# Kernel tuning notes

Measured on AMD Instinct MI355X. Metric: run time of the kernel, lower is better.

Reference implementation:

```python
import jax, jax.numpy as jnp
import numpy as np

SH_DEGREE = 1
D_SH = (SH_DEGREE + 1) ** 2  # 4
SCALE_MIN = 0.5
SCALE_MAX = 15.0
MULTIPLIER = 0.1
EPS = 1e-8


def quat_to_rotmat(q):
    # q: [..., 4] (w, x, y, z), assumed (near-)normalized
    w, x, y, z = q[..., 0], q[..., 1], q[..., 2], q[..., 3]
    return jnp.stack([
        jnp.stack([1 - 2 * (y * y + z * z), 2 * (x * y - w * z), 2 * (x * z + w * y)], -1),
        jnp.stack([2 * (x * y + w * z), 1 - 2 * (x * x + z * z), 2 * (y * z - w * x)], -1),
        jnp.stack([2 * (x * z - w * y), 2 * (y * z + w * x), 1 - 2 * (x * x + y * y)], -1),
    ], -2)


def setup_inputs() -> dict:
    key = jax.random.key(0)
    ks = jax.random.split(key, 6)
    B, N = 8, 131072
    H, W = 256, 512
    # valid SE(3) extrinsics (rotation from random unit quaternion)
    q = jax.random.normal(ks[0], (B, 1, 4), dtype=jnp.float32)
    q = q / jnp.linalg.norm(q, axis=-1, keepdims=True)
    R = quat_to_rotmat(q)
    t = jax.random.normal(ks[1], (B, 1, 3), dtype=jnp.float32)
    ext = jnp.zeros((B, 1, 4, 4), jnp.float32)
    ext = ext.at[..., :3, :3].set(R).at[..., :3, 3].set(t).at[..., 3, 3].set(1.0)
    # normalized pinhole intrinsics
    K = jnp.array([[1.2, 0.0, 0.5], [0.0, 1.2, 0.5], [0.0, 0.0, 1.0]], jnp.float32)
    K = jnp.broadcast_to(K, (B, 1, 3, 3))
    coordinates = jax.random.uniform(ks[2], (B, N, 2), dtype=jnp.float32)
    depths = jax.random.uniform(ks[3], (B, N), dtype=jnp.float32, minval=0.5, maxval=10.0)
    opacities = jax.random.uniform(ks[4], (B, N), dtype=jnp.float32)
    raw_gaussians = jax.random.normal(ks[5], (B, N, 7 + 3 * D_SH), dtype=jnp.float32)
    return {"extrinsics": ext, "intrinsics": K, "coordinates": coordinates,
            "depths": depths, "opacities": opacities, "raw_gaussians": raw_gaussians,
            "h": H, "w": W}


def reference(extrinsics, intrinsics, coordinates, depths, opacities, raw_gaussians, h, w):
    # sh mask: degree-0 untouched, degree d scaled by 0.1 * 0.25**d
    sh_mask = jnp.ones((D_SH,), jnp.float32)
    for d in range(1, SH_DEGREE + 1):
        sh_mask = sh_mask.at[d ** 2:(d + 1) ** 2].set(0.1 * 0.25 ** d)

    scales_raw = raw_gaussians[..., :3]
    rot_raw = raw_gaussians[..., 3:7]
    sh = raw_gaussians[..., 7:]

    scales = SCALE_MIN + (SCALE_MAX - SCALE_MIN) * jax.nn.sigmoid(scales_raw)

    # scale multiplier from inverse of 2x2 top-left of intrinsics
    pixel_size = 1.0 / jnp.array([w, h], jnp.float32)
    a = intrinsics[..., 0, 0]; b = intrinsics[..., 0, 1]
    c = intrinsics[..., 1, 0]; d = intrinsics[..., 1, 1]
    det = a * d - b * c
    inv2 = jnp.stack([jnp.stack([d, -b], -1), jnp.stack([-c, a], -1)], -2) / det[..., None, None]
    multiplier = (MULTIPLIER * jnp.einsum('...ij,j->...i', inv2, pixel_size)).sum(-1)  # [B,1]

    scales = scales * depths[..., None] * multiplier[..., None]  # [B,N,3]

    rotations = rot_raw / (jnp.linalg.norm(rot_raw, axis=-1, keepdims=True) + EPS)  # [B,N,4]

    sh = sh.reshape(*sh.shape[:-1], 3, D_SH) * sh_mask  # [B,N,3,D_SH]

    # covariance = R diag(s^2) R^T, then rotate into world frame
    R = quat_to_rotmat(rotations)  # [B,N,3,3]
    cov = jnp.einsum('...ij,...j,...kj->...ik', R, scales * scales, R)
    c2w = extrinsics[..., :3, :3]  # [B,1,3,3]
    cov = jnp.einsum('...ij,...jk,...lk->...il', c2w, cov, c2w)  # [B,N,3,3]

    # world rays: unproject pixel coords with depth 1, normalize, rotate to world
    coords_h = jnp.concatenate([coordinates, jnp.ones_like(coordinates[..., :1])], -1)  # [B,N,3]
    Kinv = jnp.linalg.inv(intrinsics)  # [B,1,3,3]
    dirs = jnp.einsum('...ij,...j->...i', Kinv, coords_h)
    dirs = dirs / jnp.linalg.norm(dirs, axis=-1, keepdims=True)
    dirs_w = jnp.einsum('...ij,...j->...i', c2w, dirs)  # [B,N,3]
    origins = jnp.broadcast_to(extrinsics[..., :3, 3], dirs_w.shape)
    means = origins + dirs_w * depths[..., None]  # [B,N,3]

    # rotate SH: l=0 identity; l=1 Wigner-D equals c2w in the (y,z,x) permuted basis
    p = jnp.array([1, 2, 0])
    D1 = c2w[..., p, :][..., :, p]  # [B,1,3,3]
    sh0 = sh[..., :1]
    sh1 = jnp.einsum('...ij,...cj->...ci', D1, sh[..., 1:4])
    harmonics = jnp.concatenate([sh0, sh1], -1)  # [B,N,3,D_SH]

    rotations_b = jnp.broadcast_to(rotations, (*scales.shape[:-1], 4))
    return (means, cov, harmonics, opacities, scales, rotations_b)
```

## Files before the change

kernel.cpp:

```cpp
#include <hip/hip_runtime.h>
#include <math.h>

#define SCALE_MIN 0.5f
#define SCALE_MAX 15.0f
#define MULTIPLIER 0.1f
#define EPS 1e-8f

typedef float v4f __attribute__((ext_vector_type(4)));
typedef float v2f __attribute__((ext_vector_type(2)));


#define WVF 1216
#define A_MEAN  0
#define A_COV   192
#define A_SCALE 768

__global__ __launch_bounds__(256, 4) void mono_gaussian_adapter_kernel(
    const float* __restrict__ ext,
    const float* __restrict__ intr,
    const float* __restrict__ coord,
    const float* __restrict__ depth,
    const float* __restrict__ opac,
    const float* __restrict__ rawg,
    const int* __restrict__ hp,
    const int* __restrict__ wp,
    float* __restrict__ out,
    int bpb,
    int BN)
{
    __shared__ __align__(16) float lds[4 * WVF];

    const int tid  = threadIdx.x;
    const int lane = tid & 63;
    const int wid  = tid >> 6;
    const int blk  = blockIdx.x;
    const int gid  = blk * 256 + tid;
    const int gw   = blk * 4 + wid;
    const int b    = blk / bpb;

    float* lw = lds + wid * WVF;

    {
        const v4f* gsrc = (const v4f*)(rawg + (long long)gw * (64 * 19));
        #pragma unroll
        for (int i = 0; i < 4; ++i) {
            __builtin_amdgcn_global_load_lds(
                (const __attribute__((address_space(1))) void*)(gsrc + i * 64 + lane),
                (__attribute__((address_space(3))) void*)((v4f*)lw + i * 64),
                16, 0, 0);
        }
        if (lane < 48) {
            __builtin_amdgcn_global_load_lds(
                (const __attribute__((address_space(1))) void*)(gsrc + 256 + lane),
                (__attribute__((address_space(3))) void*)((v4f*)lw + 256),
                16, 0, 0);
        }
    }

    v2f uv  = __builtin_nontemporal_load((const v2f*)coord + gid);
    float dep = __builtin_nontemporal_load(depth + gid);
    float op  = __builtin_nontemporal_load(opac + gid);

    float inv_w = 1.0f / (float)wp[0];
    float inv_h = 1.0f / (float)hp[0];

    const float* E = ext + b * 16;
    float c00=E[0],  c01=E[1],  c02=E[2],  t0=E[3];
    float c10=E[4],  c11=E[5],  c12=E[6],  t1=E[7];
    float c20=E[8],  c21=E[9],  c22=E[10], t2=E[11];

    const float* Kb = intr + b * 9;
    float k00=Kb[0],k01=Kb[1],k02=Kb[2];
    float k10=Kb[3],k11=Kb[4],k12=Kb[5];
    float k20=Kb[6],k21=Kb[7],k22=Kb[8];

    float det2 = k00*k11 - k01*k10;
    float mult = MULTIPLIER * ((k11*inv_w - k01*inv_h) + (k00*inv_h - k10*inv_w)) / det2;

    float det3 = k00*(k11*k22 - k12*k21)
               + k01*(k12*k20 - k10*k22)
               + k02*(k10*k21 - k11*k20);
    float id3 = 1.0f / det3;
    float i00 = (k11*k22 - k12*k21)*id3;
    float i01 = (k02*k21 - k01*k22)*id3;
    float i02 = (k01*k12 - k02*k11)*id3;
    float i10 = (k12*k20 - k10*k22)*id3;
    float i11 = (k00*k22 - k02*k20)*id3;
    float i12 = (k02*k10 - k00*k12)*id3;
    float i20 = (k10*k21 - k11*k20)*id3;
    float i21 = (k01*k20 - k00*k21)*id3;
    float i22 = (k00*k11 - k01*k10)*id3;

    asm volatile("s_waitcnt vmcnt(0)" ::: "memory");

    const float* g = lw + lane * 19;
    float sr0 = g[0], sr1 = g[1], sr2 = g[2];
    float q0 = g[3], q1 = g[4], q2 = g[5], q3 = g[6];
    float sh00=g[7],  sh01=g[8],  sh02=g[9],  sh03=g[10];
    float sh10=g[11], sh11=g[12], sh12=g[13], sh13=g[14];
    float sh20=g[15], sh21=g[16], sh22=g[17], sh23=g[18];

    float s0 = SCALE_MIN + (SCALE_MAX - SCALE_MIN) / (1.0f + __expf(-sr0));
    float s1 = SCALE_MIN + (SCALE_MAX - SCALE_MIN) / (1.0f + __expf(-sr1));
    float s2 = SCALE_MIN + (SCALE_MAX - SCALE_MIN) / (1.0f + __expf(-sr2));
    float dm = dep * mult;
    s0 *= dm; s1 *= dm; s2 *= dm;

    float qn = sqrtf(q0*q0 + q1*q1 + q2*q2 + q3*q3) + EPS;
    float qi = 1.0f / qn;
    float qw = q0*qi, qx = q1*qi, qy = q2*qi, qz = q3*qi;

    __builtin_nontemporal_store(op, out + 24LL*BN + gid);
    v4f rq = { qw, qx, qy, qz };
    __builtin_nontemporal_store(rq, (v4f*)(out + 28LL*BN) + gid);

    float r00 = 1.0f - 2.0f*(qy*qy + qz*qz);
    float r01 = 2.0f*(qx*qy - qw*qz);
    float r02 = 2.0f*(qx*qz + qw*qy);
    float r10 = 2.0f*(qx*qy + qw*qz);
    float r11 = 1.0f - 2.0f*(qx*qx + qz*qz);
    float r12 = 2.0f*(qy*qz - qw*qx);
    float r20 = 2.0f*(qx*qz - qw*qy);
    float r21 = 2.0f*(qy*qz + qw*qx);
    float r22 = 1.0f - 2.0f*(qx*qx + qy*qy);

    float v0 = s0*s0, v1 = s1*s1, v2 = s2*s2;
    float p00 = r00*r00*v0 + r01*r01*v1 + r02*r02*v2;
    float p01 = r00*r10*v0 + r01*r11*v1 + r02*r12*v2;
    float p02 = r00*r20*v0 + r01*r21*v1 + r02*r22*v2;
    float p11 = r10*r10*v0 + r11*r11*v1 + r12*r12*v2;
    float p12 = r10*r20*v0 + r11*r21*v1 + r12*r22*v2;
    float p22 = r20*r20*v0 + r21*r21*v1 + r22*r22*v2;

    float m00 = c00*p00 + c01*p01 + c02*p02;
    float m01 = c00*p01 + c01*p11 + c02*p12;
    float m02 = c00*p02 + c01*p12 + c02*p22;
    float m10 = c10*p00 + c11*p01 + c12*p02;
    float m11 = c10*p01 + c11*p11 + c12*p12;
    float m12 = c10*p02 + c11*p12 + c12*p22;
    float m20 = c20*p00 + c21*p01 + c22*p02;
    float m21 = c20*p01 + c21*p11 + c22*p12;
    float m22 = c20*p02 + c21*p12 + c22*p22;

    float q00 = m00*c00 + m01*c01 + m02*c02;
    float q01 = m00*c10 + m01*c11 + m02*c12;
    float q02 = m00*c20 + m01*c21 + m02*c22;
    float q11 = m10*c10 + m11*c11 + m12*c12;
    float q12 = m10*c20 + m11*c21 + m12*c22;
    float q22 = m20*c20 + m21*c21 + m22*c22;

    float d0 = i00*uv.x + i01*uv.y + i02;
    float d1 = i10*uv.x + i11*uv.y + i12;
    float d2 = i20*uv.x + i21*uv.y + i22;
    float rn = rsqrtf(d0*d0 + d1*d1 + d2*d2);
    d0 *= rn; d1 *= rn; d2 *= rn;
    float w0 = c00*d0 + c01*d1 + c02*d2;
    float w1 = c10*d0 + c11*d1 + c12*d2;
    float w2 = c20*d0 + c21*d1 + c22*d2;
    float me0 = t0 + w0*dep;
    float me1 = t1 + w1*dep;
    float me2 = t2 + w2*dep;

    float D00=c11, D01=c12, D02=c10;
    float D10=c21, D11=c22, D12=c20;
    float D20=c01, D21=c02, D22=c00;
    const float msk = 0.1f * 0.25f;
    float a1 = msk*sh01, a2 = msk*sh02, a3 = msk*sh03;
    float b1 = msk*sh11, b2 = msk*sh12, b3 = msk*sh13;
    float e1 = msk*sh21, e2 = msk*sh22, e3 = msk*sh23;
    v4f h0 = { sh00, D00*a1 + D01*a2 + D02*a3,
                     D10*a1 + D11*a2 + D12*a3,
                     D20*a1 + D21*a2 + D22*a3 };
    v4f h1 = { sh10, D00*b1 + D01*b2 + D02*b3,
                     D10*b1 + D11*b2 + D12*b3,
                     D20*b1 + D21*b2 + D22*b3 };
    v4f h2 = { sh20, D00*e1 + D01*e2 + D02*e3,
                     D10*e1 + D11*e2 + D12*e3,
                     D20*e1 + D21*e2 + D22*e3 };

    {
        float* lm = lw + A_MEAN + lane * 3;
        lm[0] = me0; lm[1] = me1; lm[2] = me2;

        float* lc = lw + A_COV + lane * 9;
        lc[0]=q00; lc[1]=q01; lc[2]=q02;
        lc[3]=q01; lc[4]=q11; lc[5]=q12;
        lc[6]=q02; lc[7]=q12; lc[8]=q22;

        float* ls = lw + A_SCALE + lane * 3;
        ls[0] = s0; ls[1] = s1; ls[2] = s2;
    }
    {
        const v4f* l4 = (const v4f*)lw;
        v4f* gm = (v4f*)(out + (long long)gw * 192);
        v4f* gs = (v4f*)(out + 25LL*BN + (long long)gw * 192);
        if (lane < 48) {
            __builtin_nontemporal_store(l4[(A_MEAN / 4) + lane], gm + lane);
            __builtin_nontemporal_store(l4[(A_SCALE / 4) + lane], gs + lane);
        }
        v4f* gc = (v4f*)(out + 3LL*BN + (long long)gw * 576);
        #pragma unroll
        for (int i = 0; i < 2; ++i)
            __builtin_nontemporal_store(l4[(A_COV / 4) + lane + i*64], gc + lane + i*64);
        if (lane < 16)
            __builtin_nontemporal_store(l4[(A_COV / 4) + lane + 128], gc + lane + 128);
    }

    {
        v4f* lh = (v4f*)lw + lane * 3;
        lh[0] = h0; lh[1] = h1; lh[2] = h2;
    }
    {
        const v4f* l4 = (const v4f*)lw;
        v4f* gh = (v4f*)(out + 12LL*BN + (long long)gw * 768);
        #pragma unroll
        for (int i = 0; i < 3; ++i)
            __builtin_nontemporal_store(l4[lane + i*64], gh + lane + i*64);
    }
}

extern "C" void kernel_launch(void* const* d_in, const int* in_sizes, int n_in,
                              void* d_out, int out_size, void* d_ws, size_t ws_size,
                              hipStream_t stream) {
    const float* ext   = (const float*)d_in[0];
    const float* intr  = (const float*)d_in[1];
    const float* coord = (const float*)d_in[2];
    const float* depth = (const float*)d_in[3];
    const float* opac  = (const float*)d_in[4];
    const float* rawg  = (const float*)d_in[5];
    const int*   hp    = (const int*)d_in[6];
    const int*   wp    = (const int*)d_in[7];

    int BN = in_sizes[3];
    int B  = in_sizes[0] / 16;
    int N  = BN / B;
    int blocks = BN / 256;
    int bpb = N / 256;

    mono_gaussian_adapter_kernel<<<blocks, 256, 0, stream>>>(
        ext, intr, coord, depth, opac, rawg, hp, wp,
        (float*)d_out, bpb, BN);
}
```

Baseline: 216.8 us.

## Load raw gaussians through registers and stage all outputs in one LDS pass

Replaces the direct global-to-LDS async loads with nontemporal vector loads into registers that are then written to LDS. It also enlarges the per-wave LDS region so harmonics get their own slot, letting all outputs be written to LDS before a single store phase instead of reusing the buffer in two phases. Launch bounds drop the min-blocks hint. The larger LDS footprint per block may lower occupancy, and the register staging adds VGPR pressure and extra LDS write instructions.

```diff
diff --git a/kernel.cpp b/kernel.cpp
--- a/kernel.cpp
+++ b/kernel.cpp
@@ -10,12 +10,13 @@
 typedef float v2f __attribute__((ext_vector_type(2)));
 
 
-#define WVF 1216
-#define A_MEAN  0
-#define A_COV   192
-#define A_SCALE 768
-
-__global__ __launch_bounds__(256, 4) void mono_gaussian_adapter_kernel(
+#define WVF 1728
+#define O_MEAN  0
+#define O_COV   192
+#define O_HARM  768
+#define O_SCALE 1536
+
+__global__ __launch_bounds__(256) void mono_gaussian_adapter_kernel(
     const float* __restrict__ ext,
     const float* __restrict__ intr,
     const float* __restrict__ coord,
@@ -40,22 +41,13 @@
 
     float* lw = lds + wid * WVF;
 
-    {
-        const v4f* gsrc = (const v4f*)(rawg + (long long)gw * (64 * 19));
-        #pragma unroll
-        for (int i = 0; i < 4; ++i) {
-            __builtin_amdgcn_global_load_lds(
-                (const __attribute__((address_space(1))) void*)(gsrc + i * 64 + lane),
-                (__attribute__((address_space(3))) void*)((v4f*)lw + i * 64),
-                16, 0, 0);
-        }
-        if (lane < 48) {
-            __builtin_amdgcn_global_load_lds(
-                (const __attribute__((address_space(1))) void*)(gsrc + 256 + lane),
-                (__attribute__((address_space(3))) void*)((v4f*)lw + 256),
-                16, 0, 0);
-        }
-    }
+    const v4f* gin = (const v4f*)(rawg + (long long)gw * (64 * 19));
+    v4f s0v = __builtin_nontemporal_load(gin + lane);
+    v4f s1v = __builtin_nontemporal_load(gin + 64 + lane);
+    v4f s2v = __builtin_nontemporal_load(gin + 128 + lane);
+    v4f s3v = __builtin_nontemporal_load(gin + 192 + lane);
+    v4f s4v;
+    if (lane < 48) s4v = __builtin_nontemporal_load(gin + 256 + lane);
 
     v2f uv  = __builtin_nontemporal_load((const v2f*)coord + gid);
     float dep = __builtin_nontemporal_load(depth + gid);
@@ -91,7 +83,14 @@
     float i21 = (k01*k20 - k00*k21)*id3;
     float i22 = (k00*k11 - k01*k10)*id3;
 
-    asm volatile("s_waitcnt vmcnt(0)" ::: "memory");
+    {
+        v4f* l4 = (v4f*)lw;
+        l4[lane]       = s0v;
+        l4[64 + lane]  = s1v;
+        l4[128 + lane] = s2v;
+        l4[192 + lane] = s3v;
+        if (lane < 48) l4[256 + lane] = s4v;
+    }
 
     const float* g = lw + lane * 19;
     float sr0 = g[0], sr1 = g[1], sr2 = g[2];
@@ -179,43 +178,40 @@
                      D20*e1 + D21*e2 + D22*e3 };
 
     {
-        float* lm = lw + A_MEAN + lane * 3;
+        float* lm = lw + O_MEAN + lane * 3;
         lm[0] = me0; lm[1] = me1; lm[2] = me2;
 
-        float* lc = lw + A_COV + lane * 9;
+        float* lc = lw + O_COV + lane * 9;
         lc[0]=q00; lc[1]=q01; lc[2]=q02;
         lc[3]=q01; lc[4]=q11; lc[5]=q12;
         lc[6]=q02; lc[7]=q12; lc[8]=q22;
 
-        float* ls = lw + A_SCALE + lane * 3;
+        v4f* lh = (v4f*)(lds + (wid * WVF + O_HARM)) + lane * 3;
+        lh[0] = h0; lh[1] = h1; lh[2] = h2;
+
+        float* ls = lw + O_SCALE + lane * 3;
         ls[0] = s0; ls[1] = s1; ls[2] = s2;
     }
+
     {
         const v4f* l4 = (const v4f*)lw;
         v4f* gm = (v4f*)(out + (long long)gw * 192);
         v4f* gs = (v4f*)(out + 25LL*BN + (long long)gw * 192);
         if (lane < 48) {
-            __builtin_nontemporal_store(l4[(A_MEAN / 4) + lane], gm + lane);
-            __builtin_nontemporal_store(l4[(A_SCALE / 4) + lane], gs + lane);
+            __builtin_nontemporal_store(l4[(O_MEAN / 4) + lane], gm + lane);
+            __builtin_nontemporal_store(l4[(O_SCALE / 4) + lane], gs + lane);
         }
         v4f* gc = (v4f*)(out + 3LL*BN + (long long)gw * 576);
         #pragma unroll
         for (int i = 0; i < 2; ++i)
-            __builtin_nontemporal_store(l4[(A_COV / 4) + lane + i*64], gc + lane + i*64);
+            __builtin_nontemporal_store(l4[(O_COV / 4) + lane + i*64], gc + lane + i*64);
         if (lane < 16)
-            __builtin_nontemporal_store(l4[(A_COV / 4) + lane + 128], gc + lane + 128);
-    }
-
-    {
-        v4f* lh = (v4f*)lw + lane * 3;
-        lh[0] = h0; lh[1] = h1; lh[2] = h2;
-    }
-    {
-        const v4f* l4 = (const v4f*)lw;
+            __builtin_nontemporal_store(l4[(O_COV / 4) + lane + 128], gc + lane + 128);
+
         v4f* gh = (v4f*)(out + 12LL*BN + (long long)gw * 768);
         #pragma unroll
         for (int i = 0; i < 3; ++i)
-            __builtin_nontemporal_store(l4[lane + i*64], gh + lane + i*64);
+            __builtin_nontemporal_store(l4[(O_HARM / 4) + lane + i*64], gh + lane + i*64);
     }
 }
 
```

New measurement: 212.6 us. Within noise of the previous version (-1.9%).
